# Optimization experiments

Measured on AMD Instinct MI355X. Metric: run time of the kernel, lower is better.

Reference implementation:

```python
import jax, jax.numpy as jnp
import numpy as np

B, T, ENC_DIM, DEC_DIM = 64, 2048, 1024, 1024


def setup_inputs() -> dict:
    key = jax.random.key(0)
    k1, k2, k3, k4, k5 = jax.random.split(key, 5)
    enc_out = jax.random.normal(k1, (B, T, ENC_DIM), dtype=jnp.float32)
    dec_state = jax.random.normal(k2, (B, DEC_DIM), dtype=jnp.float32)
    # nn.Linear(enc_dim+dec_dim, dec_dim): weight [dec_dim, enc_dim+dec_dim], bias [dec_dim]
    fan_in = ENC_DIM + DEC_DIM
    bound = 1.0 / np.sqrt(fan_in)
    W_weight = jax.random.uniform(k3, (DEC_DIM, fan_in), minval=-bound, maxval=bound, dtype=jnp.float32)
    W_bias = jax.random.uniform(k4, (DEC_DIM,), minval=-bound, maxval=bound, dtype=jnp.float32)
    # nn.Linear(dec_dim, 1, bias=False): weight [1, dec_dim]
    bound_v = 1.0 / np.sqrt(DEC_DIM)
    v_weight = jax.random.uniform(k5, (1, DEC_DIM), minval=-bound_v, maxval=bound_v, dtype=jnp.float32)
    return {"enc_out": enc_out, "dec_state": dec_state, "W_weight": W_weight, "W_bias": W_bias, "v_weight": v_weight}


def reference(enc_out, dec_state, W_weight, W_bias, v_weight):
    enc_dim = enc_out.shape[-1]
    # split W over the concat axis: cat([enc_out, dec_state]) @ W.T == enc_out @ We.T + dec_state @ Wd.T
    We = W_weight[:, :enc_dim]   # [dec_dim, enc_dim]
    Wd = W_weight[:, enc_dim:]   # [dec_dim, dec_dim]
    # [B,T,dec_dim] + [B,1,dec_dim] broadcast (avoids repeat/concat materialization)
    energy = jnp.tanh(
        jnp.einsum('bte,de->btd', enc_out, We)
        + (jnp.einsum('bd,ed->be', dec_state, Wd) + W_bias)[:, None, :]
    )
    scores = jnp.einsum('btd,d->bt', energy, v_weight[0])  # [B,T]
    alpha = jax.nn.softmax(scores, axis=1)
    context = jnp.einsum('bte,bt->be', enc_out, alpha)     # [B,enc_dim]
    return context
```

## Files before the change

kernel.cpp:

```cpp
#include <hip/hip_runtime.h>
#include <hip/hip_bf16.h>
#include <cmath>

#define BB 64
#define TT 2048
#define EE 1024
#define DD 1024
#define FAN 2048

typedef __attribute__((ext_vector_type(8))) short bhalf8;
typedef __attribute__((ext_vector_type(4))) float fvec4;

#define OFF_WE   0u
#define OFF_C    2097152u
#define OFF_SP   2359296u
#define OFF_A    4456448u
#define OFF_P    4980736u

__device__ __forceinline__ short f2bf(float f) {
    unsigned int u = __float_as_uint(f);
    u += 0x7FFFu + ((u >> 16) & 1u);
    return (short)(u >> 16);
}

__device__ __forceinline__ bhalf8 cvt8(float4 a, float4 b) {
    bhalf8 h;
    h[0] = f2bf(a.x); h[1] = f2bf(a.y); h[2] = f2bf(a.z); h[3] = f2bf(a.w);
    h[4] = f2bf(b.x); h[5] = f2bf(b.y); h[6] = f2bf(b.z); h[7] = f2bf(b.w);
    return h;
}

__device__ __forceinline__ float fast_tanhf(float x) {
    float ax = __builtin_fabsf(x);
    float e  = __expf(-2.0f * ax);
    float r  = (1.0f - e) * __builtin_amdgcn_rcpf(1.0f + e);
    return __builtin_copysignf(r, x);
}

__global__ void prep_we_k(const float* __restrict__ W, short* __restrict__ wsWe) {
    int g  = blockIdx.x * 256 + threadIdx.x;
    int ec = g >> 12;
    int eo = (g >> 10) & 3;
    int d  = g & 1023;
    const float* src = W + (size_t)d * FAN + ec * 32 + eo * 8;
    float4 f0 = *(const float4*)src;
    float4 f1 = *(const float4*)(src + 4);
    *(bhalf8*)((char*)wsWe + (size_t)ec * 65536 + eo * 16384 + d * 16) = cvt8(f0, f1);
}

__global__ void prep_c_k(const float* __restrict__ W, const float* __restrict__ bias,
                         const float* __restrict__ dec, float* __restrict__ cbuf) {
    int wg   = blockIdx.x * 4 + (threadIdx.x >> 6);
    int lane = threadIdx.x & 63;
    int b = wg >> 10, d = wg & 1023;
    const float* wrow = W + (size_t)d * FAN + EE;
    const float* drow = dec + b * DD;
    float p = 0.f;
#pragma unroll
    for (int i = 0; i < 16; ++i)
        p += wrow[i * 64 + lane] * drow[i * 64 + lane];
#pragma unroll
    for (int off = 1; off < 64; off <<= 1)
        p += __shfl_xor(p, off);
    if (lane == 0) cbuf[b * DD + d] = p + bias[d];
}

__global__ __launch_bounds__(512, 4)
void scores_k(const float* __restrict__ enc, const short* __restrict__ wsWe,
              const float* __restrict__ cbuf, const float* __restrict__ vw,
              float* __restrict__ sp) {
    __shared__ short sA[2][4][128][8];
    __shared__ float sRed[8][64];

    const int tid  = threadIdx.x;
    const int w    = tid >> 6;
    const int wm   = w >> 2;
    const int wn   = w & 3;
    const int lane = tid & 63;
    const int lrow = lane >> 4;
    const int lcol = lane & 15;
    const int b  = blockIdx.y;
    const int tt = blockIdx.x >> 2;
    const int dq = blockIdx.x & 3;
    const int t0 = tt * 128;

    const int st  = tid >> 2;
    const int seo = tid & 3;
    const int stw = st ^ (seo << 2);
    const float* gsrc = enc + ((size_t)(b * TT + t0 + st)) * EE + seo * 8;

    fvec4 acc[4][4];
#pragma unroll
    for (int m = 0; m < 4; ++m)
#pragma unroll
        for (int n = 0; n < 4; ++n)
            acc[m][n] = (fvec4){0.f, 0.f, 0.f, 0.f};

    const char* Bbase = (const char*)wsWe + lrow * 16384
                      + (size_t)(dq * 256 + wn * 64 + lcol) * 16;

    {
        float4 x0 = *(const float4*)(gsrc);
        float4 x1 = *(const float4*)(gsrc + 4);
        *(bhalf8*)&sA[0][seo][stw][0] = cvt8(x0, x1);
    }
    __syncthreads();

#pragma unroll 2
    for (int i = 0; i < 32; ++i) {
        const int buf = i & 1;
        float4 x0, x1;
        if (i < 31) {
            x0 = *(const float4*)(gsrc + (i + 1) * 32);
            x1 = *(const float4*)(gsrc + (i + 1) * 32 + 4);
        }
        bhalf8 bf[4];
#pragma unroll
        for (int n = 0; n < 4; ++n)
            bf[n] = *(const bhalf8*)(Bbase + (size_t)i * 65536 + n * 256);
        bhalf8 af[4];
#pragma unroll
        for (int m = 0; m < 4; ++m) {
            int t = wm * 64 + m * 16 + lcol;
            af[m] = *(const bhalf8*)&sA[buf][lrow][t ^ (lrow << 2)][0];
        }
#pragma unroll
        for (int n = 0; n < 4; ++n)
#pragma unroll
            for (int m = 0; m < 4; ++m)
                acc[m][n] = __builtin_amdgcn_mfma_f32_16x16x32_bf16(af[m], bf[n], acc[m][n], 0, 0, 0);
        if (i < 31)
            *(bhalf8*)&sA[buf ^ 1][seo][stw][0] = cvt8(x0, x1);
        __syncthreads();
    }

    float cv[4], vv[4];
#pragma unroll
    for (int n = 0; n < 4; ++n) {
        int d = dq * 256 + wn * 64 + n * 16 + lcol;
        cv[n] = cbuf[b * DD + d];
        vv[n] = vw[d];
    }

#pragma unroll
    for (int m = 0; m < 4; ++m) {
#pragma unroll
        for (int j = 0; j < 4; ++j) {
            float p = 0.f;
#pragma unroll
            for (int n = 0; n < 4; ++n)
                p += vv[n] * fast_tanhf(acc[m][n][j] + cv[n]);
            p += __shfl_xor(p, 1); p += __shfl_xor(p, 2);
            p += __shfl_xor(p, 4); p += __shfl_xor(p, 8);
            if (lcol == 0) sRed[w][m * 16 + lrow * 4 + j] = p;
        }
    }
    __syncthreads();
    if (tid < 128) {
        int r  = tid;
        int rm = r >> 6, lr = r & 63;
        float v2 = sRed[rm * 4 + 0][lr] + sRed[rm * 4 + 1][lr]
                 + sRed[rm * 4 + 2][lr] + sRed[rm * 4 + 3][lr];
        sp[((size_t)dq * BB + b) * TT + t0 + r] = v2;
    }
}

__global__ void softmax_k(const float* __restrict__ sp, float* __restrict__ alpha) {
    int b = blockIdx.x, tid = threadIdx.x;
    float s[8];
    float m = -1e30f;
#pragma unroll
    for (int i = 0; i < 8; ++i) {
        size_t idx = (size_t)b * TT + i * 256 + tid;
        s[i] = sp[idx] + sp[(size_t)BB * TT + idx]
             + sp[2 * (size_t)BB * TT + idx] + sp[3 * (size_t)BB * TT + idx];
        m = fmaxf(m, s[i]);
    }
#pragma unroll
    for (int off = 1; off < 64; off <<= 1) m = fmaxf(m, __shfl_xor(m, off));
    __shared__ float red[4], red2[4];
    if ((tid & 63) == 0) red[tid >> 6] = m;
    __syncthreads();
    m = fmaxf(fmaxf(red[0], red[1]), fmaxf(red[2], red[3]));
    float sum = 0.f;
#pragma unroll
    for (int i = 0; i < 8; ++i) { s[i] = expf(s[i] - m); sum += s[i]; }
#pragma unroll
    for (int off = 1; off < 64; off <<= 1) sum += __shfl_xor(sum, off);
    if ((tid & 63) == 0) red2[tid >> 6] = sum;
    __syncthreads();
    sum = red2[0] + red2[1] + red2[2] + red2[3];
    float inv = 1.0f / sum;
#pragma unroll
    for (int i = 0; i < 8; ++i) alpha[b * TT + i * 256 + tid] = s[i] * inv;
}

__global__ void ctx_k(const float* __restrict__ enc, const float* __restrict__ alpha,
                      float* __restrict__ part) {
    int ts = blockIdx.x, b = blockIdx.y, tid = threadIdx.x;
    __shared__ float sAl[256];
    sAl[tid] = alpha[b * TT + ts * 256 + tid];
    __syncthreads();
    float4 acc = {0.f, 0.f, 0.f, 0.f};
    const float* base = enc + ((size_t)b * TT + ts * 256) * EE + tid * 4;
#pragma unroll 8
    for (int i = 0; i < 256; ++i) {
        float4 v = *(const float4*)(base + (size_t)i * EE);
        float a = sAl[i];
        acc.x += a * v.x; acc.y += a * v.y; acc.z += a * v.z; acc.w += a * v.w;
    }
    *(float4*)&part[(size_t)(ts * 64 + b) * EE + tid * 4] = acc;
}

__global__ void comb_k(const float* __restrict__ part, float* __restrict__ out) {
    int g = blockIdx.x * 256 + threadIdx.x;
    float s = 0.f;
#pragma unroll
    for (int ts = 0; ts < 8; ++ts) s += part[(size_t)ts * 65536 + g];
    out[g] = s;
}

extern "C" void kernel_launch(void* const* d_in, const int* in_sizes, int n_in,
                              void* d_out, int out_size, void* d_ws, size_t ws_size,
                              hipStream_t stream) {
    const float* enc  = (const float*)d_in[0];
    const float* dec  = (const float*)d_in[1];
    const float* W    = (const float*)d_in[2];
    const float* bias = (const float*)d_in[3];
    const float* vw   = (const float*)d_in[4];
    float* out = (float*)d_out;

    char* ws = (char*)d_ws;
    short* wsWe   = (short*)(ws + OFF_WE);
    float* cbuf   = (float*)(ws + OFF_C);
    float* sp     = (float*)(ws + OFF_SP);
    float* alpha  = (float*)(ws + OFF_A);
    float* part   = (float*)(ws + OFF_P);

    prep_we_k<<<512, 256, 0, stream>>>(W, wsWe);
    prep_c_k<<<16384, 256, 0, stream>>>(W, bias, dec, cbuf);
    scores_k<<<dim3(64, 64), 512, 0, stream>>>(enc, wsWe, cbuf, vw, sp);
    softmax_k<<<64, 256, 0, stream>>>(sp, alpha);
    ctx_k<<<dim3(8, 64), 256, 0, stream>>>(enc, alpha, part);
    comb_k<<<256, 256, 0, stream>>>(part, out);
}
```

Measured before the change: 540.8 us.

## Pre-convert encoder to bf16 and stream tiles into LDS via async DMA pipeline

Adds a pass converting enc_out to bf16 in workspace, then rewrites the scores GEMM to load A tiles with global_load_lds into a triple-buffered LDS ring, with explicit waitcnt/barrier scheduling and double-buffered B fragments. This removes the repeated fp32 loads and per-block conversion across the four d-quarter blocks, and overlaps loads with MFMA. It costs an extra full read and a half-size write of the encoder tensor, and needs a large workspace, falling back to the old kernel otherwise.

```diff
diff --git a/kernel.cpp b/kernel.cpp
--- a/kernel.cpp
+++ b/kernel.cpp
@@ -16,6 +16,8 @@
 #define OFF_SP   2359296u
 #define OFF_A    4456448u
 #define OFF_P    4980736u
+#define OFF_ENCB 8388608u
+#define WS_NEED  (OFF_ENCB + (size_t)BB * TT * EE * 2)
 
 __device__ __forceinline__ short f2bf(float f) {
     unsigned int u = __float_as_uint(f);
@@ -35,6 +37,13 @@
     float e  = __expf(-2.0f * ax);
     float r  = (1.0f - e) * __builtin_amdgcn_rcpf(1.0f + e);
     return __builtin_copysignf(r, x);
+}
+
+__device__ __forceinline__ void dma16(const void* g, void* l) {
+    __builtin_amdgcn_global_load_lds(
+        (const __attribute__((address_space(1))) void*)g,
+        (__attribute__((address_space(3))) void*)l,
+        16, 0, 0);
 }
 
 __global__ void prep_we_k(const float* __restrict__ W, short* __restrict__ wsWe) {
@@ -65,11 +74,19 @@
     if (lane == 0) cbuf[b * DD + d] = p + bias[d];
 }
 
+__global__ void prep_encb_k(const float* __restrict__ enc, short* __restrict__ encB) {
+    size_t g = (size_t)blockIdx.x * 256 + threadIdx.x;
+    const float* src = enc + g * 8;
+    float4 f0 = *(const float4*)src;
+    float4 f1 = *(const float4*)(src + 4);
+    *(bhalf8*)(encB + g * 8) = cvt8(f0, f1);
+}
+
 __global__ __launch_bounds__(512, 4)
-void scores_k(const float* __restrict__ enc, const short* __restrict__ wsWe,
+void scores_k(const short* __restrict__ encB, const short* __restrict__ wsWe,
               const float* __restrict__ cbuf, const float* __restrict__ vw,
               float* __restrict__ sp) {
-    __shared__ short sA[2][4][128][8];
+    __shared__ __align__(16) short smA[3][8192];
     __shared__ float sRed[8][64];
 
     const int tid  = threadIdx.x;
@@ -84,28 +101,179 @@
     const int dq = blockIdx.x & 3;
     const int t0 = tt * 128;
 
+    const int tJ = tid >> 3;
+    const int xg = (tid & 7) ^ (tJ & 7);
+    const char* gA = (const char*)encB + ((size_t)(b * TT + t0 + tJ)) * 2048 + xg * 16;
+
+    const char* Bbase = (const char*)wsWe + lrow * 16384
+                      + (size_t)(dq * 256 + wn * 64 + lcol) * 16;
+
+    fvec4 acc[4][4];
+#pragma unroll
+    for (int m = 0; m < 4; ++m)
+#pragma unroll
+        for (int n = 0; n < 4; ++n)
+            acc[m][n] = (fvec4){0.f, 0.f, 0.f, 0.f};
+
+    const int ax0 = ((lrow)     ^ (lcol & 7)) * 16;
+    const int ax1 = ((4 + lrow) ^ (lcol & 7)) * 16;
+    const int tb0 = (wm * 64 + lcol) * 128;
+
+    bhalf8 bfA[4], bfB[4];
+
+#define DMA_TILE(K, S)                                                        \
+    do {                                                                      \
+        dma16(gA + (size_t)(K) * 128,          (char*)smA[(S)] + tid * 16);   \
+        dma16(gA + 131072 + (size_t)(K) * 128, (char*)smA[(S)] + tid * 16 + 8192); \
+    } while (0)
+
+    DMA_TILE(0, 0);
+    DMA_TILE(1, 1);
+#pragma unroll
+    for (int n = 0; n < 4; ++n)
+        bfA[n] = *(const bhalf8*)(Bbase + n * 256);
+    asm volatile("s_waitcnt vmcnt(6)" ::: "memory");
+    __builtin_amdgcn_s_barrier();
+
+#define STEP(I, S, SS, DOSTAGE, DOPRE)                                        \
+    do {                                                                      \
+        if (DOSTAGE) DMA_TILE((I) + 2, SS);                                   \
+                                                                     \
+        {                                                                     \
+            _Pragma("unroll")                                                 \
+            for (int n = 0; n < 4; ++n)                                       \
+                bfB[n] = *(const bhalf8*)(Bbase                               \
+                          + (size_t)(2 * (I) + 1) * 65536 + n * 256);         \
+            bhalf8 af[4];                                                     \
+            _Pragma("unroll")                                                 \
+            for (int m = 0; m < 4; ++m)                                       \
+                af[m] = *(const bhalf8*)((const char*)smA[(S)]                \
+                          + tb0 + m * 2048 + ax0);                            \
+            __builtin_amdgcn_s_setprio(1);                                    \
+            _Pragma("unroll")                                                 \
+            for (int n = 0; n < 4; ++n)                                       \
+                _Pragma("unroll")                                             \
+                for (int m = 0; m < 4; ++m)                                   \
+                    acc[m][n] = __builtin_amdgcn_mfma_f32_16x16x32_bf16(      \
+                        af[m], bfA[n], acc[m][n], 0, 0, 0);                   \
+            __builtin_amdgcn_s_setprio(0);                                    \
+        }                                                                     \
+                                                                     \
+        {                                                                     \
+            if (DOPRE) {                                                      \
+                _Pragma("unroll")                                             \
+                for (int n = 0; n < 4; ++n)                                   \
+                    bfA[n] = *(const bhalf8*)(Bbase                           \
+                              + (size_t)(2 * (I) + 2) * 65536 + n * 256);     \
+            }                                                                 \
+            bhalf8 af[4];                                                     \
+            _Pragma("unroll")                                                 \
+            for (int m = 0; m < 4; ++m)                                       \
+                af[m] = *(const bhalf8*)((const char*)smA[(S)]                \
+                          + tb0 + m * 2048 + ax1);                            \
+            __builtin_amdgcn_s_setprio(1);                                    \
+            _Pragma("unroll")                                                 \
+            for (int n = 0; n < 4; ++n)                                       \
+                _Pragma("unroll")                                             \
+                for (int m = 0; m < 4; ++m)                                   \
+                    acc[m][n] = __builtin_amdgcn_mfma_f32_16x16x32_bf16(      \
+                        af[m], bfB[n], acc[m][n], 0, 0, 0);                   \
+            __builtin_amdgcn_s_setprio(0);                                    \
+        }                                                                     \
+    } while (0)
+
+#define WB(N)                                                                 \
+    do {                                                                      \
+        asm volatile("s_waitcnt vmcnt(" #N ")" ::: "memory");                 \
+        __builtin_amdgcn_s_barrier();                                         \
+    } while (0)
+
+    STEP(0, 0, 2, 1, 1);  WB(6);
+    STEP(1, 1, 0, 1, 1);  WB(6);
+    STEP(2, 2, 1, 1, 1);  WB(6);
+    STEP(3, 0, 2, 1, 1);  WB(6);
+    STEP(4, 1, 0, 1, 1);  WB(6);
+    STEP(5, 2, 1, 1, 1);  WB(6);
+    STEP(6, 0, 2, 1, 1);  WB(6);
+    STEP(7, 1, 0, 1, 1);  WB(6);
+    STEP(8, 2, 1, 1, 1);  WB(6);
+    STEP(9, 0, 2, 1, 1);  WB(6);
+    STEP(10, 1, 0, 1, 1); WB(6);
+    STEP(11, 2, 1, 1, 1); WB(6);
+    STEP(12, 0, 2, 1, 1); WB(6);
+    STEP(13, 1, 0, 1, 1); WB(6);
+    STEP(14, 2, 0, 0, 1); WB(4);
+    STEP(15, 0, 0, 0, 0);
+#undef STEP
+#undef WB
+#undef DMA_TILE
+
+    float cv[4], vv[4];
+#pragma unroll
+    for (int n = 0; n < 4; ++n) {
+        int d = dq * 256 + wn * 64 + n * 16 + lcol;
+        cv[n] = cbuf[b * DD + d];
+        vv[n] = vw[d];
+    }
+
+#pragma unroll
+    for (int m = 0; m < 4; ++m) {
+#pragma unroll
+        for (int j = 0; j < 4; ++j) {
+            float p = 0.f;
+#pragma unroll
+            for (int n = 0; n < 4; ++n)
+                p += vv[n] * fast_tanhf(acc[m][n][j] + cv[n]);
+            p += __shfl_xor(p, 1); p += __shfl_xor(p, 2);
+            p += __shfl_xor(p, 4); p += __shfl_xor(p, 8);
+            if (lcol == 0) sRed[w][m * 16 + lrow * 4 + j] = p;
+        }
+    }
+    __syncthreads();
+    if (tid < 128) {
+        int r  = tid;
+        int rm = r >> 6, lr = r & 63;
+        float v2 = sRed[rm * 4 + 0][lr] + sRed[rm * 4 + 1][lr]
+                 + sRed[rm * 4 + 2][lr] + sRed[rm * 4 + 3][lr];
+        sp[((size_t)dq * BB + b) * TT + t0 + r] = v2;
+    }
+}
+
+__global__ __launch_bounds__(512, 4)
+void scores_fb_k(const float* __restrict__ enc, const short* __restrict__ wsWe,
+                 const float* __restrict__ cbuf, const float* __restrict__ vw,
+                 float* __restrict__ sp) {
+    __shared__ short sA[2][4][128][8];
+    __shared__ float sRed[8][64];
+    const int tid  = threadIdx.x;
+    const int w    = tid >> 6;
+    const int wm   = w >> 2;
+    const int wn   = w & 3;
+    const int lane = tid & 63;
+    const int lrow = lane >> 4;
+    const int lcol = lane & 15;
+    const int b  = blockIdx.y;
+    const int tt = blockIdx.x >> 2;
+    const int dq = blockIdx.x & 3;
+    const int t0 = tt * 128;
     const int st  = tid >> 2;
     const int seo = tid & 3;
     const int stw = st ^ (seo << 2);
     const float* gsrc = enc + ((size_t)(b * TT + t0 + st)) * EE + seo * 8;
-
     fvec4 acc[4][4];
 #pragma unroll
     for (int m = 0; m < 4; ++m)
 #pragma unroll
         for (int n = 0; n < 4; ++n)
             acc[m][n] = (fvec4){0.f, 0.f, 0.f, 0.f};
-
     const char* Bbase = (const char*)wsWe + lrow * 16384
                       + (size_t)(dq * 256 + wn * 64 + lcol) * 16;
-
     {
         float4 x0 = *(const float4*)(gsrc);
         float4 x1 = *(const float4*)(gsrc + 4);
         *(bhalf8*)&sA[0][seo][stw][0] = cvt8(x0, x1);
     }
     __syncthreads();
-
 #pragma unroll 2
     for (int i = 0; i < 32; ++i) {
         const int buf = i & 1;
@@ -133,7 +301,6 @@
             *(bhalf8*)&sA[buf ^ 1][seo][stw][0] = cvt8(x0, x1);
         __syncthreads();
     }
-
     float cv[4], vv[4];
 #pragma unroll
     for (int n = 0; n < 4; ++n) {
@@ -141,7 +308,6 @@
         cv[n] = cbuf[b * DD + d];
         vv[n] = vw[d];
     }
-
 #pragma unroll
     for (int m = 0; m < 4; ++m) {
 #pragma unroll
@@ -236,10 +402,16 @@
     float* sp     = (float*)(ws + OFF_SP);
     float* alpha  = (float*)(ws + OFF_A);
     float* part   = (float*)(ws + OFF_P);
+    short* encB   = (short*)(ws + OFF_ENCB);
 
     prep_we_k<<<512, 256, 0, stream>>>(W, wsWe);
     prep_c_k<<<16384, 256, 0, stream>>>(W, bias, dec, cbuf);
-    scores_k<<<dim3(64, 64), 512, 0, stream>>>(enc, wsWe, cbuf, vw, sp);
+    if (ws_size >= WS_NEED) {
+        prep_encb_k<<<65536, 256, 0, stream>>>(enc, encB);
+        scores_k<<<dim3(64, 64), 512, 0, stream>>>(encB, wsWe, cbuf, vw, sp);
+    } else {
+        scores_fb_k<<<dim3(64, 64), 512, 0, stream>>>(enc, wsWe, cbuf, vw, sp);
+    }
     softmax_k<<<64, 256, 0, stream>>>(sp, alpha);
     ctx_k<<<dim3(8, 64), 256, 0, stream>>>(enc, alpha, part);
     comb_k<<<256, 256, 0, stream>>>(part, out);
```

Result: no change. 532.1 us (-1.6%).
